# Performance work log

Measured on AMD Instinct MI355X. Metric: run time of the kernel, lower is better.

## Reference

```python
import jax, jax.numpy as jnp
import numpy as np

C, BS1, NODE, L, K = 2, 9, 820, 3, 17  # BS1 = 1 + bs
SQRT2 = 1.4142135623730951
SQRT2PI = 2.5066282746310002
EPS = 1e-30  # fp32-safe stand-in for the 1e-307 used in the float64 original

# Gauss-Hermite quadrature points (physicists'), as in gausshermite(k, dims=[1,1,1,1,-1])
_x, _ = np.polynomial.hermite.hermgauss(K)
_XN = _x.reshape(1, 1, 1, 1, K).astype(np.float32)
_mi, _mj = np.meshgrid(_x, _x)
_XI = _mi.reshape(1, 1, 1, 1, K * K).astype(np.float32)
_XJ = _mj.reshape(1, 1, 1, 1, K * K).astype(np.float32)

# fine-to-coarse MRF edge target indices (length 819), exact tile/reshape pattern from __init__
_id1 = np.tile(np.tile(np.arange(729, 810).reshape(-1, 1), (1, 3)).reshape(-1, 1, 27), (1, 3, 1)).reshape(-1)
_id2 = np.tile(np.tile(np.arange(810, 819).reshape(-1, 1), (1, 3)).reshape(-1, 9), (1, 3)).reshape(-1)
_ID = np.concatenate([_id1, _id2, np.full(9, 819)]).astype(np.int32)


def setup_inputs() -> dict:
    key = jax.random.key(0)
    k1, k2, k3 = jax.random.split(key, 3)
    mu = jax.random.normal(k1, (C, BS1, NODE, L, 1), jnp.float32)
    sigma = jax.random.uniform(k2, (C, BS1, NODE, L, 1), jnp.float32, minval=0.1, maxval=1.0)
    w = jax.random.normal(k3, (C, BS1, 1, L, 1), jnp.float32)
    return {"mu": mu, "sigma": sigma, "w": w}


def reference(mu, sigma, w):
    xq = jnp.asarray(_XN)
    xi = jnp.asarray(_XI)
    xj = jnp.asarray(_XJ)
    ids = jnp.asarray(_ID)

    # quadrature points aligned with each mixture component's distribution
    xn = xq * sigma * SQRT2 + mu                         # (C,BS1,820,L,K)
    u1, o1 = mu[:, :, :-1], sigma[:, :, :-1]             # (C,BS1,819,L,1)
    u2, o2 = mu[:, :, ids], sigma[:, :, ids]             # gather along node axis
    x1 = xi * o1 * SQRT2 + u1                            # (C,BS1,819,L,K*K)
    x2 = xj * o2 * SQRT2 + u2
    xe = jnp.stack([x1, x2], -1)                         # (C,BS1,819,L,K*K,2)

    alpha = jax.nn.softmax(w, axis=3)                    # (C,BS1,1,L,1)
    alf = alpha[:, :, :, None]                           # (C,BS1,1,1,L,1)

    # node log marginal: mixture density at each quadrature point
    o = sigma[:, :, :, None]                             # (C,BS1,820,1,L,1)
    pn = jnp.exp(-((xn[:, :, :, :, None, :] - mu[:, :, :, None]) / o) ** 2 / 2) / (o * SQRT2PI)
    lpn = jnp.log(jnp.sum(pn * alf, 4) + EPS)            # (C,BS1,820,L,K)
    lpn = jnp.concatenate([
        jnp.concatenate([lpn[:, :1, :729], jnp.zeros_like(lpn[:, 1:, :729])], 1),
        lpn[:, :, 729:]], 2)

    # edge log marginal (product of per-endpoint densities, mixture-weighted)
    o1_, o2_ = o1[:, :, :, None], o2[:, :, :, None]      # (C,BS1,819,1,L,1)
    b1 = jnp.exp(-((x1[:, :, :, :, None, :] - u1[:, :, :, None]) / o1_) ** 2 / 2) / (o1_ * SQRT2PI)
    b1 = jnp.concatenate([
        jnp.concatenate([b1[:, :1, :729], jnp.ones_like(b1[:, 1:, :729])], 1),
        b1[:, :, 729:]], 2)
    b2 = jnp.exp(-((x2[:, :, :, :, None, :] - u2[:, :, :, None]) / o2_) ** 2 / 2) / (o2_ * SQRT2PI)
    lpe = jnp.log(jnp.sum(b1 * b2 * alf, 4) + EPS)       # (C,BS1,819,L,K*K)

    return xn, xe, lpn, lpe, alpha, o1, o2
```

## Files before the change

### kernel.cpp

```cpp
#include <hip/hip_runtime.h>

#define NC    2
#define NB    9
#define NNODE 820
#define NL    3
#define NK    17
#define G     4
#define NGB   205

#define EPSF     1e-30f
#define C_SCF    0.84932178f
#define KLPN     0.46971920f
#define KE       0.22063560f

#define OFF_XN    0LL
#define OFF_XE    752760LL
#define OFF_LPN   26315388LL
#define OFF_LPE   27068148LL
#define OFF_ALPHA 39849462LL
#define OFF_O1    39849516LL
#define OFF_O2    39893742LL

constexpr double csqrt(double v) {
    if (v <= 0.0) return 0.0;
    double y = v > 1.0 ? v : 1.0;
    for (int i = 0; i < 80; ++i) y = 0.5 * (y + v / y);
    return y;
}

struct HNodesF { float x[NK]; };

constexpr HNodesF compute_nodes() {
    const int n = NK;
    const double PIM4 = 0.7511255444649425;
    double c1[NK + 1] = {}, c2[NK + 1] = {};
    for (int j = 1; j <= n; ++j) {
        c1[j] = csqrt(2.0 / (double)j);
        c2[j] = csqrt(((double)j - 1.0) / (double)j);
    }
    const double PPC = csqrt(2.0 * (double)n);
    double xr[9] = {};
    double z = 0.0;
    for (int i = 0; i < 9; ++i) {
        if (i == 0)      z = csqrt(2.0 * n + 1.0) - 1.85575 * 0.552905;
        else if (i == 1) z -= 1.14 * 3.34327 / z;
        else if (i == 2) z = 1.86 * z - 0.86 * xr[0];
        else if (i == 3) z = 1.91 * z - 0.91 * xr[1];
        else             z = 2.0 * z - xr[i - 2];
        for (int it = 0; it < 24; ++it) {
            double p1 = PIM4, p2 = 0.0;
            for (int j = 1; j <= n; ++j) {
                double p3 = p2;
                p2 = p1;
                p1 = z * c1[j] * p2 - c2[j] * p3;
            }
            double pp = PPC * p2;
            double z1 = z;
            z = z1 - p1 / pp;
            double d = z - z1; if (d < 0.0) d = -d;
            if (d <= 3.0e-14) break;
        }
        xr[i] = z;
    }
    HNodesF f{};
    for (int i = 0; i < 9; ++i) {
        f.x[16 - i] = (float)xr[i];
        f.x[i]      = (float)(-xr[i]);
    }
    return f;
}

struct TabF { float v[289 * 2]; };
constexpr TabF make_tab() {
    HNodesF h = compute_nodes();
    TabF t{};
    for (int q = 0; q < 289; ++q) {
        t.v[2 * q]     = (float)((double)h.x[q % 17] * 1.4142135623730951);
        t.v[2 * q + 1] = (float)((double)h.x[q / 17] * 1.4142135623730951);
    }
    return t;
}
constexpr TabF TABC = make_tab();

__device__ __forceinline__ int idOf(int n) {
    if (n < 729) { return 729 + (n / 81) * 9 + (n % 27) / 3; }
    if (n < 810) { int m = n - 729; return 810 + (m / 27) * 3 + (m % 9) / 3; }
    return 819;
}

__device__ __forceinline__ float rcpf(float x) { return __builtin_amdgcn_rcpf(x); }

__global__ __launch_bounds__(256) void fused_kernel(const float* __restrict__ mu,
                                                    const float* __restrict__ sg,
                                                    const float* __restrict__ w,
                                                    float* __restrict__ out) {
    const int g   = blockIdx.x;
    const int cb  = blockIdx.y;
    const int b   = cb % NB;
    const int n0  = g * G;
    const int tid = threadIdx.x;

    __shared__ float2 tab[289];
    {
        const float2* tc = (const float2*)TABC.v;
        tab[tid] = tc[tid];
        if (tid < 33) tab[256 + tid] = tc[256 + tid];
    }

    const float* wB = w + cb * 3;
    float w0 = wB[0], w1 = wB[1], w2 = wB[2];
    float wm = fmaxf(w0, fmaxf(w1, w2));
    float e0 = __expf(w0 - wm), e1 = __expf(w1 - wm), e2 = __expf(w2 - wm);
    float ainv = 1.0f / (e0 + e1 + e2);
    float a0 = e0 * ainv, a1 = e1 * ainv, a2 = e2 * ainv;

    const size_t cbase = (size_t)cb * NNODE;

    __syncthreads();

    if (tid < 204) {
        int nn = tid / 51;
        int r  = tid - 51 * nn;
        int l1 = r / 17;
        int k  = r - 17 * l1;
        int n  = n0 + nn;
        size_t mb = (cbase + n) * 3;
        float ul = mu[mb + l1], sl = sg[mb + l1];
        float xn = fmaf(tab[k].x, sl, ul);
        out[OFF_XN + (cbase + n0) * 51 + tid] = xn;

        float lp = 0.0f;
        if (!(b >= 1 && n < 729)) {
            float ua = mu[mb], ub = mu[mb + 1], uc = mu[mb + 2];
            float ia = C_SCF * rcpf(sg[mb]);
            float ib = C_SCF * rcpf(sg[mb + 1]);
            float ic = C_SCF * rcpf(sg[mb + 2]);
            float d0 = (xn - ua) * ia;
            float d1 = (xn - ub) * ib;
            float d2 = (xn - uc) * ic;
            float sum = a0 * ia * exp2f(-(d0 * d0))
                      + a1 * ib * exp2f(-(d1 * d1))
                      + a2 * ic * exp2f(-(d2 * d2));
            lp = __logf(sum * KLPN + EPSF);
        }
        out[OFF_LPN + (cbase + n0) * 51 + tid] = lp;
    } else if (tid < 216) {
        int t = tid - 204; int nn = t / 3, c = t - 3 * nn; int n = n0 + nn;
        if (n < 819) out[OFF_O1 + ((size_t)cb * 819 + n) * 3 + c] = sg[(cbase + n) * 3 + c];
    } else if (tid < 228) {
        int t = tid - 216; int nn = t / 3, c = t - 3 * nn; int n = n0 + nn;
        if (n < 819) out[OFF_O2 + ((size_t)cb * 819 + n) * 3 + c] = sg[(cbase + idOf(n)) * 3 + c];
    }

    if (g == 0 && cb == 0 && tid < 54) {
        int cb2 = tid / 3, l = tid - 3 * cb2;
        const float* wB2 = w + cb2 * 3;
        float v0 = wB2[0], v1 = wB2[1], v2 = wB2[2];
        float vm = fmaxf(v0, fmaxf(v1, v2));
        float f0 = __expf(v0 - vm), f1 = __expf(v1 - vm), f2 = __expf(v2 - vm);
        float finv = 1.0f / (f0 + f1 + f2);
        float fl = (l == 0) ? f0 : ((l == 1) ? f1 : f2);
        out[OFF_ALPHA + tid] = fl * finv;
    }

    const int wv = tid >> 6, ln = tid & 63;
    const size_t ecb = (size_t)cb * 819;

#pragma unroll
    for (int nn = 0; nn < G; ++nn) {
        int n = n0 + nn;
        if (n >= 819) continue;
        int idn = idOf(n);
        size_t mb1 = (cbase + n) * 3, mb2 = (cbase + (size_t)idn) * 3;
        float u1a = mu[mb1], u1b = mu[mb1 + 1], u1c = mu[mb1 + 2];
        float s1a = sg[mb1], s1b = sg[mb1 + 1], s1c = sg[mb1 + 2];
        float u2a = mu[mb2], u2b = mu[mb2 + 1], u2c = mu[mb2 + 2];
        float s2a = sg[mb2], s2b = sg[mb2 + 1], s2c = sg[mb2 + 2];
        float i2a = C_SCF * rcpf(s2a), i2b = C_SCF * rcpf(s2b), i2c = C_SCF * rcpf(s2c);

        const bool mk = (b >= 1) && (n < 729);
        float i1a = 0.f, i1b = 0.f, i1c = 0.f, ca, cbv, cc;
        if (mk) {
            ca  = a0 * i2a * KLPN;
            cbv = a1 * i2b * KLPN;
            cc  = a2 * i2c * KLPN;
        } else {
            i1a = C_SCF * rcpf(s1a); i1b = C_SCF * rcpf(s1b); i1c = C_SCF * rcpf(s1c);
            ca  = a0 * i1a * i2a * KE;
            cbv = a1 * i1b * i2b * KE;
            cc  = a2 * i1c * i2c * KE;
        }

        float2* xp0 = reinterpret_cast<float2*>(out + OFF_XE) + (ecb + n) * 867;
        float*  lp0 = out + OFF_LPE + (ecb + n) * 867;

#pragma unroll
        for (int l1 = 0; l1 < 3; ++l1) {
            float u1l = (l1 == 0) ? u1a : ((l1 == 1) ? u1b : u1c);
            float s1l = (l1 == 0) ? s1a : ((l1 == 1) ? s1b : s1c);
            float u2l = (l1 == 0) ? u2a : ((l1 == 1) ? u2b : u2c);
            float s2l = (l1 == 0) ? s2a : ((l1 == 1) ? s2b : s2c);
            float2* xp = xp0 + l1 * 289;
            float*  lp = lp0 + l1 * 289;

            auto body = [&](int q) {
                float2 tv = tab[q];
                float x1 = fmaf(tv.x, s1l, u1l);
                float x2 = fmaf(tv.y, s2l, u2l);
                xp[q] = make_float2(x1, x2);
                float d0 = (x2 - u2a) * i2a;
                float d1 = (x2 - u2b) * i2b;
                float d2 = (x2 - u2c) * i2c;
                float t0 = d0 * d0, t1 = d1 * d1, t2 = d2 * d2;
                if (!mk) {
                    float f0v = (x1 - u1a) * i1a; t0 = fmaf(f0v, f0v, t0);
                    float f1v = (x1 - u1b) * i1b; t1 = fmaf(f1v, f1v, t1);
                    float f2v = (x1 - u1c) * i1c; t2 = fmaf(f2v, f2v, t2);
                }
                float sum = fmaf(cc, exp2f(-t2), fmaf(cbv, exp2f(-t1), ca * exp2f(-t0)));
                lp[q] = __logf(sum + EPSF);
            };

            body(tid);
            const int sec = nn * 3 + l1;
            if (wv == (sec & 3) && ln < 33) body(256 + ln);
        }
    }
}

extern "C" void kernel_launch(void* const* d_in, const int* in_sizes, int n_in,
                              void* d_out, int out_size, void* d_ws, size_t ws_size,
                              hipStream_t stream) {
    const float* mu    = (const float*)d_in[0];
    const float* sigma = (const float*)d_in[1];
    const float* w     = (const float*)d_in[2];
    float* out = (float*)d_out;

    hipLaunchKernelGGL(fused_kernel, dim3(NGB, NC * NB), dim3(256), 0, stream,
                       mu, sigma, w, out);
}
```

Measured before the change: 33.13 us.

## Factor edge Gaussian products into per-axis tables in shared memory

Uses the separability of the Gaussian-product edge density: per-axis factors exp(-f^2) for the first endpoint and mixture-weighted exp(-d^2) for the second endpoint are precomputed in shared memory for each node/component (17 values each). The 289-point loop then does three FMAs from shared memory instead of six exponentials. Masked nodes reuse a precomputed 17-entry log table. Per-node mu/sigma parameters are staged in shared memory. The cost is extra barriers and shared-memory traffic, and the kernel stays bound by output stores.

```diff
diff --git a/kernel.cpp b/kernel.cpp
--- a/kernel.cpp
+++ b/kernel.cpp
@@ -90,6 +90,13 @@
 
 __device__ __forceinline__ float rcpf(float x) { return __builtin_amdgcn_rcpf(x); }
 
+__device__ __forceinline__ float sel3(float a0, float a1, float a2, int i) {
+    float r = a0;
+    r = (i == 1) ? a1 : r;
+    r = (i == 2) ? a2 : r;
+    return r;
+}
+
 __global__ __launch_bounds__(256) void fused_kernel(const float* __restrict__ mu,
                                                     const float* __restrict__ sg,
                                                     const float* __restrict__ w,
@@ -101,10 +108,30 @@
     const int tid = threadIdx.x;
 
     __shared__ float2 tab[289];
+    __shared__ float  params[48];
+    __shared__ float  sCEj[612];
+    __shared__ float  sEi [612];
+    __shared__ float  sLpj[204];
+
     {
         const float2* tc = (const float2*)TABC.v;
         tab[tid] = tc[tid];
         if (tid < 33) tab[256 + tid] = tc[256 + tid];
+    }
+
+    const size_t cbase = (size_t)cb * NNODE;
+
+    if (tid < 48) {
+        int nn = tid / 12, r = tid - nn * 12;
+        int n = n0 + nn;
+        size_t b1a = (cbase + n) * 3;
+        size_t b2a = (cbase + (size_t)idOf(n)) * 3;
+        float v;
+        if (r < 3)      v = mu[b1a + r];
+        else if (r < 6) v = sg[b1a + r - 3];
+        else if (r < 9) v = mu[b2a + r - 6];
+        else            v = sg[b2a + r - 9];
+        params[tid] = v;
     }
 
     const float* wB = w + cb * 3;
@@ -113,8 +140,6 @@
     float e0 = __expf(w0 - wm), e1 = __expf(w1 - wm), e2 = __expf(w2 - wm);
     float ainv = 1.0f / (e0 + e1 + e2);
     float a0 = e0 * ainv, a1 = e1 * ainv, a2 = e2 * ainv;
-
-    const size_t cbase = (size_t)cb * NNODE;
 
     __syncthreads();
 
@@ -163,67 +188,81 @@
         out[OFF_ALPHA + tid] = fl * finv;
     }
 
+    for (int v = tid; v < 612; v += 256) {
+        int s  = v / 51, r = v - s * 51;
+        int m  = r / 17, j = r - m * 17;
+        int nn = s / 3,  l1 = s - nn * 3;
+        int n  = n0 + nn;
+        const float* P = params + nn * 12;
+        float u1l = P[l1],     s1l = P[3 + l1];
+        float u2l = P[6 + l1], s2l = P[9 + l1];
+        float u1m = P[m],      s1m = P[3 + m];
+        float u2m = P[6 + m],  s2m = P[9 + m];
+        float i2m = C_SCF * rcpf(s2m);
+        float i1m = C_SCF * rcpf(s1m);
+        float am  = sel3(a0, a1, a2, m);
+        bool  mk  = (b >= 1) && (n < 729);
+        float cm  = mk ? (am * i2m * KLPN) : (am * i1m * i2m * KE);
+        float xv  = tab[j].x;
+        float x2j = fmaf(xv, s2l, u2l);
+        float d   = (x2j - u2m) * i2m;
+        sCEj[v] = cm * exp2f(-(d * d));
+        float x1i = fmaf(xv, s1l, u1l);
+        float f   = (x1i - u1m) * i1m;
+        sEi[v]  = exp2f(-(f * f));
+    }
+    __syncthreads();
+    if (tid < 204) {
+        int s = tid / 17, j = tid - s * 17;
+        float sum = sCEj[s * 51 + j] + sCEj[s * 51 + 17 + j] + sCEj[s * 51 + 34 + j];
+        sLpj[tid] = __logf(sum + EPSF);
+    }
+    __syncthreads();
+
     const int wv = tid >> 6, ln = tid & 63;
+    const int j0 = tid / 17, i0 = tid - 17 * j0;
+    const int qt = 256 + ln;
+    const int jt = qt / 17, it = qt - 17 * jt;
     const size_t ecb = (size_t)cb * 819;
 
-#pragma unroll
     for (int nn = 0; nn < G; ++nn) {
         int n = n0 + nn;
         if (n >= 819) continue;
-        int idn = idOf(n);
-        size_t mb1 = (cbase + n) * 3, mb2 = (cbase + (size_t)idn) * 3;
-        float u1a = mu[mb1], u1b = mu[mb1 + 1], u1c = mu[mb1 + 2];
-        float s1a = sg[mb1], s1b = sg[mb1 + 1], s1c = sg[mb1 + 2];
-        float u2a = mu[mb2], u2b = mu[mb2 + 1], u2c = mu[mb2 + 2];
-        float s2a = sg[mb2], s2b = sg[mb2 + 1], s2c = sg[mb2 + 2];
-        float i2a = C_SCF * rcpf(s2a), i2b = C_SCF * rcpf(s2b), i2c = C_SCF * rcpf(s2c);
-
         const bool mk = (b >= 1) && (n < 729);
-        float i1a = 0.f, i1b = 0.f, i1c = 0.f, ca, cbv, cc;
-        if (mk) {
-            ca  = a0 * i2a * KLPN;
-            cbv = a1 * i2b * KLPN;
-            cc  = a2 * i2c * KLPN;
-        } else {
-            i1a = C_SCF * rcpf(s1a); i1b = C_SCF * rcpf(s1b); i1c = C_SCF * rcpf(s1c);
-            ca  = a0 * i1a * i2a * KE;
-            cbv = a1 * i1b * i2b * KE;
-            cc  = a2 * i1c * i2c * KE;
-        }
-
+        const float* P = params + nn * 12;
         float2* xp0 = reinterpret_cast<float2*>(out + OFF_XE) + (ecb + n) * 867;
         float*  lp0 = out + OFF_LPE + (ecb + n) * 867;
 
 #pragma unroll
         for (int l1 = 0; l1 < 3; ++l1) {
-            float u1l = (l1 == 0) ? u1a : ((l1 == 1) ? u1b : u1c);
-            float s1l = (l1 == 0) ? s1a : ((l1 == 1) ? s1b : s1c);
-            float u2l = (l1 == 0) ? u2a : ((l1 == 1) ? u2b : u2c);
-            float s2l = (l1 == 0) ? s2a : ((l1 == 1) ? s2b : s2c);
+            const int sec = nn * 3 + l1;
+            float u1l = P[l1],     s1l = P[3 + l1];
+            float u2l = P[6 + l1], s2l = P[9 + l1];
             float2* xp = xp0 + l1 * 289;
             float*  lp = lp0 + l1 * 289;
-
-            auto body = [&](int q) {
+            const float* CE = sCEj + sec * 51;
+            const float* EI = sEi  + sec * 51;
+            const float* LJ = sLpj + sec * 17;
+
+            auto body = [&](int q, int i, int j) {
                 float2 tv = tab[q];
                 float x1 = fmaf(tv.x, s1l, u1l);
                 float x2 = fmaf(tv.y, s2l, u2l);
                 xp[q] = make_float2(x1, x2);
-                float d0 = (x2 - u2a) * i2a;
-                float d1 = (x2 - u2b) * i2b;
-                float d2 = (x2 - u2c) * i2c;
-                float t0 = d0 * d0, t1 = d1 * d1, t2 = d2 * d2;
-                if (!mk) {
-                    float f0v = (x1 - u1a) * i1a; t0 = fmaf(f0v, f0v, t0);
-                    float f1v = (x1 - u1b) * i1b; t1 = fmaf(f1v, f1v, t1);
-                    float f2v = (x1 - u1c) * i1c; t2 = fmaf(f2v, f2v, t2);
+                float lv;
+                if (mk) {
+                    lv = LJ[j];
+                } else {
+                    float sum = fmaf(EI[i], CE[j],
+                                fmaf(EI[17 + i], CE[17 + j],
+                                     EI[34 + i] * CE[34 + j]));
+                    lv = __logf(sum + EPSF);
                 }
-                float sum = fmaf(cc, exp2f(-t2), fmaf(cbv, exp2f(-t1), ca * exp2f(-t0)));
-                lp[q] = __logf(sum + EPSF);
+                lp[q] = lv;
             };
 
-            body(tid);
-            const int sec = nn * 3 + l1;
-            if (wv == (sec & 3) && ln < 33) body(256 + ln);
+            body(tid, i0, j0);
+            if (wv == (sec & 3) && ln < 33) body(qt, it, jt);
         }
     }
 }
```

Result: no change. 33.60 us (+1.4%).
